# Kernel tuning notes

Measured on AMD Instinct MI355X. Metric: run time of the kernel, lower is better.

## Reference

```python
import jax, jax.numpy as jnp
import numpy as np

CHUNK = 32  # config.scan_chunk_size


def setup_inputs() -> dict:
    key = jax.random.key(0)
    ks = jax.random.split(key, 12)
    B, T, D, SD, OD = 8, 2048, 512, 256, 64
    w = lambda i, shape: (jax.random.normal(ks[i], shape, dtype=jnp.float32) * 0.02)
    return {
        "x": jax.random.normal(ks[0], (B, T, D), dtype=jnp.float32),
        "gate_W": w(1, (D, SD)), "gate_b": jnp.zeros((SD,), jnp.float32),
        "in_W": w(2, (D, SD)), "in_b": jnp.zeros((SD,), jnp.float32),
        "out_W": w(3, (SD, D)), "out_b": jnp.zeros((D,), jnp.float32),
        "opv_W": w(4, (D, OD)), "opv_b": jnp.zeros((OD,), jnp.float32),
        "opk_W": w(5, (D, OD)), "opk_b": jnp.zeros((OD,), jnp.float32),
        "opq_W": w(6, (D, OD)), "opq_b": jnp.zeros((OD,), jnp.float32),
        "op_decay": jnp.full((OD,), 0.95, jnp.float32),
        "opout_W": w(7, (OD, D)), "opout_b": jnp.zeros((D,), jnp.float32),
        "ln_g": jnp.ones((D,), jnp.float32), "ln_b": jnp.zeros((D,), jnp.float32),
    }


def _chunked_scan(gates, drive, K):
    # gates, drive: [B,T,SD]; T divisible by K
    B, T, SD = drive.shape
    nC = T // K
    a = gates.reshape(B, nC, K, SD)
    b = drive.reshape(B, nC, K, SD)
    log_cum_a = jnp.cumsum(jnp.log(jnp.maximum(a, 1e-6)), axis=2)
    cum_a = jnp.exp(log_cum_a)                               # [B,nC,K,SD]
    cum_wb = jnp.cumsum(b / jnp.maximum(cum_a, 1e-8), axis=2)
    # sequential scan over chunks to propagate the carry h
    def step(h, inputs):
        ca_last, wb_last = inputs                            # [B,SD] each
        h_new = ca_last * (h + wb_last)
        return h_new, h                                      # emit h BEFORE this chunk
    h0 = jnp.zeros((B, SD), drive.dtype)
    _, h_prev = jax.lax.scan(
        step, h0,
        (cum_a[:, :, -1].transpose(1, 0, 2), cum_wb[:, :, -1].transpose(1, 0, 2)))
    h_prev = h_prev.transpose(1, 0, 2)                       # [B,nC,SD]
    states = cum_a * (h_prev[:, :, None, :] + cum_wb)
    return states.reshape(B, T, SD)


def _binding_scan_outer(v, k, q, decay):
    # v,k,q: [B,T,OD]; S_t = diag(decay) @ S_{t-1} + v_t k_t^T; o_t = S_t q_t
    B, T, OD = v.shape
    def step(S, vkq):
        vt, kt, qt = vkq                                     # [B,OD] each
        S_new = decay[None, :, None] * S + vt[:, :, None] * kt[:, None, :]
        o = jnp.einsum('bij,bj->bi', S_new, qt)
        return S_new, o
    S0 = jnp.zeros((B, OD, OD), v.dtype)
    _, outs = jax.lax.scan(step, S0, (v.transpose(1, 0, 2), k.transpose(1, 0, 2), q.transpose(1, 0, 2)))
    return outs.transpose(1, 0, 2)                           # [B,T,OD]


def reference(x, gate_W, gate_b, in_W, in_b, out_W, out_b,
              opv_W, opv_b, opk_W, opk_b, opq_W, opq_b, op_decay,
              opout_W, opout_b, ln_g, ln_b):
    gates = jax.nn.sigmoid(x @ gate_W + gate_b)              # [B,T,SD]
    drive = (1.0 - gates) * (x @ in_W + in_b)
    states = _chunked_scan(gates, drive, CHUNK)
    scan_out = states @ out_W + out_b                        # [B,T,D]
    # binding scan (mode='outer')
    v = x @ opv_W + opv_b
    k = x @ opk_W + opk_b
    q = x @ opq_W + opq_b
    dec = jax.nn.sigmoid(op_decay)
    bind = _binding_scan_outer(v, k, q, dec) @ opout_W + opout_b
    y = x + scan_out + bind
    mu = jnp.mean(y, axis=-1, keepdims=True)
    var = jnp.mean((y - mu) ** 2, axis=-1, keepdims=True)
    return (y - mu) / jnp.sqrt(var + 1e-5) * ln_g + ln_b
```

## Files before the change

### kernel.cpp

```cpp
#include <hip/hip_runtime.h>
#include <hip/hip_bf16.h>
#include <hip/hip_fp16.h>
#include <math.h>

#define BB 8
#define TT 2048
#define DD 512
#define SD 256
#define OD 64
#define CHUNK 32
#define NC 64
#define CB 64
#define NCB 32
#define MM (BB*TT)
#define KCAT 320

typedef __attribute__((ext_vector_type(8))) short bf16x8_t;
typedef __attribute__((ext_vector_type(4))) float f32x4;

__device__ __forceinline__ void gload_lds16(const void* gsrc, void* ldst) {
    __builtin_amdgcn_global_load_lds(
        (const __attribute__((address_space(1))) unsigned int*)gsrc,
        (__attribute__((address_space(3))) unsigned int*)ldst,
        16, 0, 0);
}

__device__ __forceinline__ float4 ldh4(const __half* p) {
    __half2 a = *(const __half2*)p;
    __half2 b = *(const __half2*)(p + 2);
    float2 fa = __half22float2(a), fb = __half22float2(b);
    return make_float4(fa.x, fa.y, fb.x, fb.y);
}

__global__ __launch_bounds__(256) void conv_w(
    const float* __restrict__ gate_W, const float* __restrict__ gate_b,
    const float* __restrict__ in_W,   const float* __restrict__ in_b,
    const float* __restrict__ opv_W,  const float* __restrict__ opk_W,
    const float* __restrict__ opq_W,
    const float* __restrict__ opv_b,  const float* __restrict__ opk_b,
    const float* __restrict__ opq_b,
    __hip_bfloat16* __restrict__ Wcat, float* __restrict__ bias_cat)
{
    int idx = blockIdx.x * 256 + threadIdx.x;
    if (idx < 393216) {
        int n = idx >> 9, k = idx & 511;
        float v;
        if (n < 256)       v = gate_W[k * 256 + n];
        else if (n < 512)  v = in_W[k * 256 + (n - 256)];
        else if (n < 704) {
            int h = (n - 512) >> 6, j = (n - 512) & 63;
            const float* W = (h == 0) ? opv_W : (h == 1) ? opk_W : opq_W;
            v = W[k * 64 + j];
        } else v = 0.f;
        Wcat[idx] = __float2bfloat16(v);
        return;
    }
    idx -= 393216;
    if (idx < 768) {
        float v;
        if (idx < 256)      v = gate_b[idx];
        else if (idx < 512) v = in_b[idx - 256];
        else if (idx < 704) {
            int h = (idx - 512) >> 6, j = (idx - 512) & 63;
            v = (h == 0) ? opv_b[j] : (h == 1) ? opk_b[j] : opq_b[j];
        } else v = 0.f;
        bias_cat[idx] = v;
    }
}

__global__ __launch_bounds__(512, 6) void gemm_proj(
    const float* __restrict__ A,
    const __hip_bfloat16* __restrict__ Bt,
    const float* __restrict__ bias,
    __half* __restrict__ out0,
    __half* __restrict__ out1,
    int M, int N, int K, int n0, int sigCols)
{
    constexpr int BM = 128, BK = 32;
    __shared__ alignas(16) __hip_bfloat16 Abuf[3][BM * BK];
    __shared__ alignas(16) __hip_bfloat16 Bbuf[3][BM * BK];
    const int tid = threadIdx.x;
    const int lane = tid & 63, wid = tid >> 6;
    const int wr = wid >> 2, wc = wid & 3;
    const int nbn = N >> 7;
    const int chunk = gridDim.x >> 3;
    const int b = blockIdx.x;
    const int orig = (b & 7) * chunk + (b >> 3);
    const int bm = (orig / nbn) * BM, bn = (orig % nbn) * BM;
    const int l15 = lane & 15, hgr = lane >> 4;

    const int grow = tid >> 2, gslot = tid & 3;
    const int gsw = gslot ^ ((grow >> 1) & 3);
    const float* srcA = A + (size_t)(bm + grow) * K + gslot * 8;
    const int wOffA = grow * 64 + gsw * 16;
    const __hip_bfloat16* srcB = Bt + (size_t)(bn + grow) * K + gsw * 8;
    const int ldsOffB = (tid & ~63) * 16;

    int offA[4], offB[2];
    #pragma unroll
    for (int mi = 0; mi < 4; ++mi) {
        int r = wr * 64 + mi * 16 + l15;
        offA[mi] = r * 64 + (hgr ^ ((r >> 1) & 3)) * 16;
    }
    #pragma unroll
    for (int nj = 0; nj < 2; ++nj) {
        int r = wc * 32 + nj * 16 + l15;
        offB[nj] = r * 64 + (hgr ^ ((r >> 1) & 3)) * 16;
    }

    f32x4 acc[4][2] = {};
    const int nk = K / BK;
    float4 pA0, pA1, qA0, qA1;

#define WRITE_A(IDX, R0, R1) do { \
        alignas(16) __hip_bfloat16 h_[8] = { \
            __float2bfloat16((R0).x), __float2bfloat16((R0).y), \
            __float2bfloat16((R0).z), __float2bfloat16((R0).w), \
            __float2bfloat16((R1).x), __float2bfloat16((R1).y), \
            __float2bfloat16((R1).z), __float2bfloat16((R1).w)}; \
        *(float4*)((char*)&Abuf[(IDX)][0] + wOffA) = *(float4*)h_; \
    } while (0)

#define FRAG_MFMA(T) do { \
        const char* ab_ = (const char*)&Abuf[(T) % 3][0]; \
        const char* bb_ = (const char*)&Bbuf[(T) % 3][0]; \
        bf16x8_t af_[4], bf_[2]; \
        _Pragma("unroll") \
        for (int mi = 0; mi < 4; ++mi) af_[mi] = *(const bf16x8_t*)(ab_ + offA[mi]); \
        _Pragma("unroll") \
        for (int nj = 0; nj < 2; ++nj) bf_[nj] = *(const bf16x8_t*)(bb_ + offB[nj]); \
        _Pragma("unroll") \
        for (int mi = 0; mi < 4; ++mi) \
            _Pragma("unroll") \
            for (int nj = 0; nj < 2; ++nj) \
                acc[mi][nj] = __builtin_amdgcn_mfma_f32_16x16x32_bf16( \
                    af_[mi], bf_[nj], acc[mi][nj], 0, 0, 0); \
    } while (0)

#define GEMM_STEP(T, I0, I1, W0, W1) do { \
        int k2_ = ((T) + 2) * BK; \
        I0 = *(const float4*)(srcA + k2_); \
        I1 = *(const float4*)(srcA + k2_ + 4); \
        gload_lds16(srcB + k2_, (char*)&Bbuf[((T) + 2) % 3][0] + ldsOffB); \
        FRAG_MFMA(T); \
        WRITE_A(((T) + 1) % 3, W0, W1); \
        asm volatile("s_waitcnt vmcnt(3) lgkmcnt(0)" ::: "memory"); \
        __builtin_amdgcn_sched_barrier(0); \
        __builtin_amdgcn_s_barrier(); \
        __builtin_amdgcn_sched_barrier(0); \
    } while (0)

    pA0 = *(const float4*)(srcA);
    pA1 = *(const float4*)(srcA + 4);
    gload_lds16(srcB, (char*)&Bbuf[0][0] + ldsOffB);
    qA0 = *(const float4*)(srcA + BK);
    qA1 = *(const float4*)(srcA + BK + 4);
    gload_lds16(srcB + BK, (char*)&Bbuf[1][0] + ldsOffB);
    asm volatile("s_waitcnt vmcnt(3)" ::: "memory");
    WRITE_A(0, pA0, pA1);
    asm volatile("s_waitcnt lgkmcnt(0)" ::: "memory");
    __builtin_amdgcn_sched_barrier(0);
    __builtin_amdgcn_s_barrier();
    __builtin_amdgcn_sched_barrier(0);

    for (int tt = 0; tt + 3 < nk; tt += 2) {
        GEMM_STEP(tt,     pA0, pA1, qA0, qA1);
        GEMM_STEP(tt + 1, qA0, qA1, pA0, pA1);
    }
    FRAG_MFMA(nk - 2);
    WRITE_A((nk - 1) % 3, qA0, qA1);
    __syncthreads();
    FRAG_MFMA(nk - 1);

#undef GEMM_STEP
#undef FRAG_MFMA
#undef WRITE_A

    const int n1 = N - n0;
    #pragma unroll
    for (int mi = 0; mi < 4; ++mi) {
        #pragma unroll
        for (int nj = 0; nj < 2; ++nj) {
            int col = bn + wc * 32 + nj * 16 + l15;
            int r0 = bm + wr * 64 + mi * 16 + hgr * 4;
            float bv = bias[col];
            #pragma unroll
            for (int e = 0; e < 4; ++e) {
                int row = r0 + e;
                float val = acc[mi][nj][e] + bv;
                if (col < n0) {
                    if (col < sigCols) val = 1.f / (1.f + expf(-val));
                    out0[(size_t)row * n0 + col] = __float2half(val);
                } else {
                    out1[(size_t)row * n1 + (col - n0)] = __float2half(val);
                }
            }
        }
    }
}

__device__ void scan_pass1_body(int blk,
    const __half* __restrict__ gi,
    float* __restrict__ ca_last, float* __restrict__ wb_last)
{
    int idx = blk * 256 + threadIdx.x;
    int sd = idx & 255;
    int c  = (idx >> 8) & 63;
    int b  = idx >> 14;
    size_t base = ((size_t)(b * TT + c * CHUNK)) * 512;
    float prod = 1.f, wb = 0.f;
    for (int i = 0; i < CHUNK; ++i) {
        size_t off = base + (size_t)i * 512;
        float g  = __half2float(gi[off + sd]);
        float il = __half2float(gi[off + 256 + sd]);
        float a = fmaxf(g, 1e-6f);
        prod *= a;
        wb += (1.f - g) * il / fmaxf(prod, 1e-8f);
    }
    int cidx = (b * NC + c) * SD + sd;
    ca_last[cidx] = prod;
    wb_last[cidx] = wb;
}

__device__ void scan_pass3_body(int blk,
    const __half* __restrict__ gi, const float* __restrict__ h_prev,
    __hip_bfloat16* __restrict__ cat)
{
    int idx = blk * 256 + threadIdx.x;
    int sd = idx & 255;
    int c  = (idx >> 8) & 63;
    int b  = idx >> 14;
    size_t base = ((size_t)(b * TT + c * CHUNK)) * 512;
    size_t obase = ((size_t)(b * TT + c * CHUNK)) * KCAT + sd;
    float h = h_prev[(b * NC + c) * SD + sd];
    float prod = 1.f, wb = 0.f;
    for (int i = 0; i < CHUNK; ++i) {
        size_t off = base + (size_t)i * 512;
        float g  = __half2float(gi[off + sd]);
        float il = __half2float(gi[off + 256 + sd]);
        float a = fmaxf(g, 1e-6f);
        prod *= a;
        wb += (1.f - g) * il / fmaxf(prod, 1e-8f);
        cat[obase + (size_t)i * KCAT] = __float2bfloat16(prod * (h + wb));
    }
}

#define LST 68
__device__ void bind_p1_body(int bc,
    const __half* __restrict__ vkq, const float* __restrict__ op_decay,
    float* __restrict__ o, float* __restrict__ dS,
    float* B1, float* B2, float* B3, float* l2d)
{
    const int b = bc >> 5, c = bc & 31;
    const size_t base = ((size_t)b * TT + (size_t)c * CB) * 256;
    const size_t obase = ((size_t)b * TT + (size_t)c * CB) * OD;
    const int tid = threadIdx.x;
    if (tid < 64) l2d[tid] = log2f(1.f / (1.f + expf(-op_decay[tid])));
    const int lr = tid >> 4, lc = (tid & 15) << 2;
    #pragma unroll
    for (int rr = 0; rr < 4; ++rr) {
        int t = lr + rr * 16;
        float4 qv = ldh4(&vkq[base + t * 256 + 128 + lc]);
        float4 kv = ldh4(&vkq[base + t * 256 + 64 + lc]);
        float q4[4] = {qv.x, qv.y, qv.z, qv.w};
        float k4[4] = {kv.x, kv.y, kv.z, kv.w};
        #pragma unroll
        for (int j = 0; j < 4; ++j) {
            B1[(lc + j) * LST + t] = q4[j];
            B2[(lc + j) * LST + t] = k4[j];
        }
    }
    __syncthreads();
    const int tx = tid & 15, ty = tid >> 4;
    {
        float a_acc[4][4] = {};
        for (int d = 0; d < 64; ++d) {
            float4 q4 = *(const float4*)&B1[d * LST + 4 * ty];
            float4 k4 = *(const float4*)&B2[d * LST + 4 * tx];
            float qr[4] = {q4.x, q4.y, q4.z, q4.w};
            float kr[4] = {k4.x, k4.y, k4.z, k4.w};
            #pragma unroll
            for (int r = 0; r < 4; ++r)
                #pragma unroll
                for (int s = 0; s < 4; ++s)
                    a_acc[r][s] = fmaf(qr[r], kr[s], a_acc[r][s]);
        }
        __syncthreads();
        #pragma unroll
        for (int s = 0; s < 4; ++s) {
            int ss = 4 * tx + s;
            float w[4];
            #pragma unroll
            for (int r = 0; r < 4; ++r)
                w[r] = (ss <= 4 * ty + r) ? a_acc[r][s] : 0.f;
            *(float4*)&B3[ss * LST + 4 * ty] = *(float4*)w;
        }
    }
    #pragma unroll
    for (int rr = 0; rr < 4; ++rr) {
        int m = lr + rr * 16;
        float4 vv = ldh4(&vkq[base + m * 256 + 0 + lc]);
        float4 kv = ldh4(&vkq[base + m * 256 + 64 + lc]);
        float v4[4] = {vv.x, vv.y, vv.z, vv.w};
        #pragma unroll
        for (int j = 0; j < 4; ++j)
            v4[j] *= exp2f(-(float)m * l2d[lc + j]);
        *(float4*)&B1[m * LST + lc] = *(float4*)v4;
        float k4[4] = {kv.x, kv.y, kv.z, kv.w};
        *(float4*)&B2[m * LST + lc] = *(float4*)k4;
    }
    __syncthreads();
    {
        float p[4][4] = {};
        for (int s = 0; s < 64; ++s) {
            float4 a4 = *(const float4*)&B3[s * LST + 4 * ty];
            float4 v4 = *(const float4*)&B1[s * LST + 4 * tx];
            float ar[4] = {a4.x, a4.y, a4.z, a4.w};
            float vr[4] = {v4.x, v4.y, v4.z, v4.w};
            #pragma unroll
            for (int r = 0; r < 4; ++r)
                #pragma unroll
                for (int i2 = 0; i2 < 4; ++i2)
                    p[r][i2] = fmaf(ar[r], vr[i2], p[r][i2]);
        }
        #pragma unroll
        for (int r = 0; r < 4; ++r) {
            int t = 4 * ty + r;
            float w[4];
            #pragma unroll
            for (int i2 = 0; i2 < 4; ++i2)
                w[i2] = exp2f((float)t * l2d[4 * tx + i2]) * p[r][i2];
            *(float4*)&o[obase + t * OD + 4 * tx] = *(float4*)w;
        }
    }
    {
        float sacc[4][4] = {};
        for (int m = 0; m < 64; ++m) {
            float4 v4 = *(const float4*)&B1[m * LST + 4 * ty];
            float4 k4 = *(const float4*)&B2[m * LST + 4 * tx];
            float vr[4] = {v4.x, v4.y, v4.z, v4.w};
            float kr[4] = {k4.x, k4.y, k4.z, k4.w};
            #pragma unroll
            for (int r = 0; r < 4; ++r)
                #pragma unroll
                for (int j = 0; j < 4; ++j)
                    sacc[r][j] = fmaf(vr[r], kr[j], sacc[r][j]);
        }
        float* dSb = dS + (size_t)bc * 4096;
        #pragma unroll
        for (int r = 0; r < 4; ++r) {
            int i = 4 * ty + r;
            float scale = exp2f(63.f * l2d[i]);
            float w[4];
            #pragma unroll
            for (int j2 = 0; j2 < 4; ++j2)
                w[j2] = scale * sacc[r][j2];
            *(float4*)&dSb[i * 64 + 4 * tx] = *(float4*)w;
        }
    }
}

__device__ void bind_p3_body(int bc,
    const __half* __restrict__ vkq, const float* __restrict__ Sstart,
    const float* __restrict__ op_decay, const float* __restrict__ o,
    __hip_bfloat16* __restrict__ cat,
    float* B1, float* B2, float* l2d)
{
    const int b = bc >> 5, c = bc & 31;
    const size_t base = ((size_t)b * TT + (size_t)c * CB) * 256;
    const size_t obase = ((size_t)b * TT + (size_t)c * CB) * OD;
    const size_t cbase = ((size_t)b * TT + (size_t)c * CB) * KCAT + 256;
    const int tid = threadIdx.x;
    if (tid < 64) l2d[tid] = log2f(1.f / (1.f + expf(-op_decay[tid])));
    const int lr = tid >> 4, lc = (tid & 15) << 2;
    const float* Sb = Sstart + (size_t)bc * 4096;
    #pragma unroll
    for (int rr = 0; rr < 4; ++rr) {
        int t = lr + rr * 16;
        float4 qv = ldh4(&vkq[base + t * 256 + 128 + lc]);
        float4 sv = *(const float4*)&Sb[t * 64 + lc];
        float q4[4] = {qv.x, qv.y, qv.z, qv.w};
        float s4[4] = {sv.x, sv.y, sv.z, sv.w};
        #pragma unroll
        for (int j = 0; j < 4; ++j) {
            B1[(lc + j) * LST + t] = q4[j];
            B2[(lc + j) * LST + t] = s4[j];
        }
    }
    __syncthreads();
    const int tx = tid & 15, ty = tid >> 4;
    float acc[4][4] = {};
    for (int j = 0; j < 64; ++j) {
        float4 q4 = *(const float4*)&B1[j * LST + 4 * ty];
        float4 s4 = *(const float4*)&B2[j * LST + 4 * tx];
        float qr[4] = {q4.x, q4.y, q4.z, q4.w};
        float sr[4] = {s4.x, s4.y, s4.z, s4.w};
        #pragma unroll
        for (int r = 0; r < 4; ++r)
            #pragma unroll
            for (int i2 = 0; i2 < 4; ++i2)
                acc[r][i2] = fmaf(qr[r], sr[i2], acc[r][i2]);
    }
    #pragma unroll
    for (int r = 0; r < 4; ++r) {
        int l = 4 * ty + r;
        alignas(8) __hip_bfloat16 w[4];
        #pragma unroll
        for (int i2 = 0; i2 < 4; ++i2) {
            int i = 4 * tx + i2;
            float val = o[obase + l * OD + i] + exp2f((float)(l + 1) * l2d[i]) * acc[r][i2];
            w[i2] = __float2bfloat16(val);
        }
        *(float2*)&cat[cbase + l * KCAT + 4 * tx] = *(float2*)w;
    }
}

__global__ __launch_bounds__(256) void fused1(
    const __half* __restrict__ gi, const __half* __restrict__ vkq,
    const float* __restrict__ op_decay,
    float* __restrict__ ca_last, float* __restrict__ wb_last,
    float* __restrict__ o_intra, float* __restrict__ dS)
{
    __shared__ float B1[64 * LST];
    __shared__ float B2[64 * LST];
    __shared__ float B3[64 * LST];
    __shared__ float l2d[64];
    const int bid = blockIdx.x;
    if (bid < 256) bind_p1_body(bid, vkq, op_decay, o_intra, dS, B1, B2, B3, l2d);
    else           scan_pass1_body(bid - 256, gi, ca_last, wb_last);
}

__global__ __launch_bounds__(256) void fused2(
    const float* __restrict__ dS, const float* __restrict__ op_decay,
    float* __restrict__ Sstart,
    const float* __restrict__ ca_last, const float* __restrict__ wb_last,
    float* __restrict__ h_prev,
    const float* __restrict__ out_W, const float* __restrict__ out_b,
    const float* __restrict__ opout_W, const float* __restrict__ opout_b,
    __hip_bfloat16* __restrict__ Wcomb, float* __restrict__ bias_comb)
{
    const int bid = blockIdx.x;
    if (bid < 128) {
        int idx = bid * 256 + threadIdx.x;
        int j = idx & 63, i = (idx >> 6) & 63, b = idx >> 12;
        float dec = 1.f / (1.f + expf(-op_decay[i]));
        float d64 = exp2f(64.f * log2f(dec));
        float S = 0.f;
        for (int c = 0; c < NCB; ++c) {
            size_t o = (((size_t)b * NCB + c) * 4096) + i * 64 + j;
            Sstart[o] = S;
            S = d64 * S + dS[o];
        }
    } else if (bid < 136) {
        int idx = (bid - 128) * 256 + threadIdx.x;
        int sd = idx & 255;
        int b  = idx >> 8;
        float h = 0.f;
        for (int c = 0; c < NC; ++c) {
            int o = (b * NC + c) * SD + sd;
            h_prev[o] = h;
            h = ca_last[o] * (h + wb_last[o]);
        }
    } else {
        int idx = (bid - 136) * 256 + threadIdx.x;
        if (idx < 163840) {
            int n = idx / KCAT, k = idx % KCAT;
            float v = (k < 256) ? out_W[k * 512 + n] : opout_W[(k - 256) * 512 + n];
            Wcomb[idx] = __float2bfloat16(v);
            return;
        }
        idx -= 163840;
        if (idx < 512) bias_comb[idx] = out_b[idx] + opout_b[idx];
    }
}

__global__ __launch_bounds__(256) void fused3(
    const __half* __restrict__ gi, const float* __restrict__ h_prev,
    const __half* __restrict__ vkq, const float* __restrict__ Sstart,
    const float* __restrict__ op_decay, const float* __restrict__ o_intra,
    __hip_bfloat16* __restrict__ cat)
{
    __shared__ float B1[64 * LST];
    __shared__ float B2[64 * LST];
    __shared__ float l2d[64];
    const int bid = blockIdx.x;
    if (bid < 256) bind_p3_body(bid, vkq, Sstart, op_decay, o_intra, cat, B1, B2, l2d);
    else           scan_pass3_body(bid - 256, gi, h_prev, cat);
}

__global__ __launch_bounds__(512) void outgemm_ln(
    const __hip_bfloat16* __restrict__ cat,
    const __hip_bfloat16* __restrict__ Wcomb,
    const float* __restrict__ bias_comb,
    const float* __restrict__ x,
    const float* __restrict__ lng, const float* __restrict__ lnb,
    float* __restrict__ y)
{
    constexpr int BM = 32, BK = 32, NN = 512;
    __shared__ alignas(16) __hip_bfloat16 As[2][BM * BK];
    __shared__ alignas(16) __hip_bfloat16 Bs[2][NN * BK];
    __shared__ float psum[8][BM], psum2[8][BM], mvmu[BM], mvrs[BM];
    const int tid = threadIdx.x;
    const int lane = tid & 63, wid = tid >> 6;
    const int l15 = lane & 15, hgr = lane >> 4;
    const int bm = blockIdx.x * BM;

    const __hip_bfloat16* srcA = cat;
    int ldsOffA = 0;
    {
        int gg = (wid & 1) * 64 + lane;
        int row = gg >> 2, sl = (gg & 3) ^ ((row >> 1) & 3);
        srcA = cat + (size_t)(bm + row) * KCAT + sl * 8;
        ldsOffA = (wid & 1) * 1024;
    }
    const __hip_bfloat16* srcB[4];
    int ldsOffB[4];
    #pragma unroll
    for (int c = 0; c < 4; ++c) {
        int gg = (wid * 4 + c) * 64 + lane;
        int row = gg >> 2, sl = (gg & 3) ^ ((row >> 1) & 3);
        srcB[c] = Wcomb + (size_t)row * KCAT + sl * 8;
        ldsOffB[c] = (wid * 4 + c) * 1024;
    }
    int offA[2], offB[4];
    #pragma unroll
    for (int mi = 0; mi < 2; ++mi) {
        int r = mi * 16 + l15;
        offA[mi] = r * 64 + (hgr ^ ((r >> 1) & 3)) * 16;
    }
    #pragma unroll
    for (int nj = 0; nj < 4; ++nj) {
        int n = wid * 64 + nj * 16 + l15;
        offB[nj] = n * 64 + (hgr ^ ((n >> 1) & 3)) * 16;
    }

    f32x4 acc[2][4] = {};
    constexpr int nk = KCAT / BK;

    if (wid < 2) gload_lds16(srcA, (char*)&As[0][0] + ldsOffA);
    #pragma unroll
    for (int c = 0; c < 4; ++c) gload_lds16(srcB[c], (char*)&Bs[0][0] + ldsOffB[c]);
    __syncthreads();

    int cur = 0;
    for (int t = 0; t < nk; ++t) {
        if (t + 1 < nk) {
            int k0 = (t + 1) * BK;
            if (wid < 2) gload_lds16(srcA + k0, (char*)&As[cur ^ 1][0] + ldsOffA);
            #pragma unroll
            for (int c = 0; c < 4; ++c)
                gload_lds16(srcB[c] + k0, (char*)&Bs[cur ^ 1][0] + ldsOffB[c]);
        }
        bf16x8_t af[2], bfr[4];
        #pragma unroll
        for (int mi = 0; mi < 2; ++mi)
            af[mi] = *(const bf16x8_t*)((const char*)&As[cur][0] + offA[mi]);
        #pragma unroll
        for (int nj = 0; nj < 4; ++nj)
            bfr[nj] = *(const bf16x8_t*)((const char*)&Bs[cur][0] + offB[nj]);
        #pragma unroll
        for (int mi = 0; mi < 2; ++mi)
            #pragma unroll
            for (int nj = 0; nj < 4; ++nj)
                acc[mi][nj] = __builtin_amdgcn_mfma_f32_16x16x32_bf16(
                    af[mi], bfr[nj], acc[mi][nj], 0, 0, 0);
        __syncthreads();
        cur ^= 1;
    }

    #pragma unroll
    for (int nj = 0; nj < 4; ++nj) {
        int col = wid * 64 + nj * 16 + l15;
        float bc_ = bias_comb[col];
        #pragma unroll
        for (int mi = 0; mi < 2; ++mi) {
            int r0 = bm + mi * 16 + hgr * 4;
            #pragma unroll
            for (int e = 0; e < 4; ++e)
                acc[mi][nj][e] += bc_ + x[(size_t)(r0 + e) * DD + col];
        }
    }
    float s[8], s2[8];
    #pragma unroll
    for (int mi = 0; mi < 2; ++mi)
        #pragma unroll
        for (int e = 0; e < 4; ++e) {
            float a = 0.f, b2 = 0.f;
            #pragma unroll
            for (int nj = 0; nj < 4; ++nj) {
                float v = acc[mi][nj][e];
                a += v; b2 += v * v;
            }
            s[mi * 4 + e] = a; s2[mi * 4 + e] = b2;
        }
    #pragma unroll
    for (int off = 1; off <= 8; off <<= 1)
        #pragma unroll
        for (int i = 0; i < 8; ++i) {
            s[i]  += __shfl_xor(s[i], off);
            s2[i] += __shfl_xor(s2[i], off);
        }
    if (l15 == 0) {
        #pragma unroll
        for (int mi = 0; mi < 2; ++mi)
            #pragma unroll
            for (int e = 0; e < 4; ++e) {
                int lr = mi * 16 + hgr * 4 + e;
                psum[wid][lr]  = s[mi * 4 + e];
                psum2[wid][lr] = s2[mi * 4 + e];
            }
    }
    __syncthreads();
    if (tid < BM) {
        float tot = 0.f, tot2 = 0.f;
        #pragma unroll
        for (int w2 = 0; w2 < 8; ++w2) { tot += psum[w2][tid]; tot2 += psum2[w2][tid]; }
        float mu = tot * (1.f / 512.f);
        float var = tot2 * (1.f / 512.f) - mu * mu;
        mvmu[tid] = mu;
        mvrs[tid] = rsqrtf(var + 1e-5f);
    }
    __syncthreads();
    #pragma unroll
    for (int nj = 0; nj < 4; ++nj) {
        int col = wid * 64 + nj * 16 + l15;
        float g = lng[col], bb = lnb[col];
        #pragma unroll
        for (int mi = 0; mi < 2; ++mi) {
            #pragma unroll
            for (int e = 0; e < 4; ++e) {
                int lr = mi * 16 + hgr * 4 + e;
                y[(size_t)(bm + lr) * DD + col] =
                    (acc[mi][nj][e] - mvmu[lr]) * mvrs[lr] * g + bb;
            }
        }
    }
}

extern "C" void kernel_launch(void* const* d_in, const int* in_sizes, int n_in,
                              void* d_out, int out_size, void* d_ws, size_t ws_size,
                              hipStream_t stream)
{
    const float* x       = (const float*)d_in[0];
    const float* gate_W  = (const float*)d_in[1];
    const float* gate_b  = (const float*)d_in[2];
    const float* in_W    = (const float*)d_in[3];
    const float* in_b    = (const float*)d_in[4];
    const float* out_W   = (const float*)d_in[5];
    const float* out_b   = (const float*)d_in[6];
    const float* opv_W   = (const float*)d_in[7];
    const float* opv_b   = (const float*)d_in[8];
    const float* opk_W   = (const float*)d_in[9];
    const float* opk_b   = (const float*)d_in[10];
    const float* opq_W   = (const float*)d_in[11];
    const float* opq_b   = (const float*)d_in[12];
    const float* op_dec  = (const float*)d_in[13];
    const float* opout_W = (const float*)d_in[14];
    const float* opout_b = (const float*)d_in[15];
    const float* ln_g    = (const float*)d_in[16];
    const float* ln_b    = (const float*)d_in[17];
    float* y = (float*)d_out;

    char* w = (char*)d_ws;
    auto alloc = [&](size_t bytes) { char* p = w; w += (bytes + 255) & ~(size_t)255; return p; };
    __half* gi       = (__half*)alloc((size_t)MM * 512 * 2);
    __half* vkq      = (__half*)alloc((size_t)MM * 256 * 2);
    float* o_intra   = (float*)alloc((size_t)MM * 64 * 4);
    float* ca_last   = (float*)alloc((size_t)BB * NC * SD * 4);
    float* wb_last   = (float*)alloc((size_t)BB * NC * SD * 4);
    float* h_prev    = (float*)alloc((size_t)BB * NC * SD * 4);
    float* dS        = (float*)alloc((size_t)BB * NCB * 4096 * 4);
    float* Sstart    = (float*)alloc((size_t)BB * NCB * 4096 * 4);
    float* bias_cat  = (float*)alloc(768 * 4);
    float* bias_comb = (float*)alloc(512 * 4);
    __hip_bfloat16* cat   = (__hip_bfloat16*)alloc((size_t)MM * KCAT * 2);
    __hip_bfloat16* Wcat  = (__hip_bfloat16*)alloc((size_t)768 * 512 * 2);
    __hip_bfloat16* Wcomb = (__hip_bfloat16*)alloc((size_t)512 * KCAT * 2);

    hipLaunchKernelGGL(conv_w, dim3((393216 + 768 + 255) / 256), dim3(256), 0, stream,
                       gate_W, gate_b, in_W, in_b, opv_W, opk_W, opq_W,
                       opv_b, opk_b, opq_b, Wcat, bias_cat);
    hipLaunchKernelGGL(gemm_proj, dim3(6 * (MM / 128)), dim3(512), 0, stream,
                       x, Wcat, bias_cat, gi, vkq,
                       MM, 768, 512, 512, 256);
    hipLaunchKernelGGL(fused1, dim3(768), dim3(256), 0, stream,
                       gi, vkq, op_dec, ca_last, wb_last, o_intra, dS);
    hipLaunchKernelGGL(fused2, dim3(136 + (163840 + 512 + 255) / 256), dim3(256), 0, stream,
                       dS, op_dec, Sstart, ca_last, wb_last, h_prev,
                       out_W, out_b, opout_W, opout_b, Wcomb, bias_comb);
    hipLaunchKernelGGL(fused3, dim3(768), dim3(256), 0, stream,
                       gi, h_prev, vkq, Sstart, op_dec, o_intra, cat);
    hipLaunchKernelGGL(outgemm_ln, dim3(MM / 32), dim3(512), 0, stream,
                       cat, Wcomb, bias_comb, x, ln_g, ln_b, y);
}
```

Measured before the change: 87.61 us.

## Deepen gemm_proj prefetch pipeline to three tiles ahead with four B buffers

Restructures the projection GEMM's software pipeline so global loads are issued three K-tiles ahead instead of two. B now uses a 4-deep LDS ring and A a 2-deep ring, with a third register pair holding prefetched A. The loop is hardcoded for nk=16 (K=512) and the waitcnt thresholds are adjusted. The aim is to hide more global-memory latency, at the cost of more LDS and registers, which may reduce occupancy. It also breaks generality for other K values.

```diff
diff --git a/kernel.cpp b/kernel.cpp
--- a/kernel.cpp
+++ b/kernel.cpp
@@ -77,8 +77,8 @@
     int M, int N, int K, int n0, int sigCols)
 {
     constexpr int BM = 128, BK = 32;
-    __shared__ alignas(16) __hip_bfloat16 Abuf[3][BM * BK];
-    __shared__ alignas(16) __hip_bfloat16 Bbuf[3][BM * BK];
+    __shared__ alignas(16) __hip_bfloat16 Abuf[2][BM * BK];
+    __shared__ alignas(16) __hip_bfloat16 Bbuf[4][BM * BK];
     const int tid = threadIdx.x;
     const int lane = tid & 63, wid = tid >> 6;
     const int wr = wid >> 2, wc = wid & 3;
@@ -110,7 +110,7 @@
 
     f32x4 acc[4][2] = {};
     const int nk = K / BK;
-    float4 pA0, pA1, qA0, qA1;
+    float4 pA0, pA1, qA0, qA1, rA0, rA1;
 
 #define WRITE_A(IDX, R0, R1) do { \
         alignas(16) __hip_bfloat16 h_[8] = { \
@@ -122,8 +122,8 @@
     } while (0)
 
 #define FRAG_MFMA(T) do { \
-        const char* ab_ = (const char*)&Abuf[(T) % 3][0]; \
-        const char* bb_ = (const char*)&Bbuf[(T) % 3][0]; \
+        const char* ab_ = (const char*)&Abuf[(T) & 1][0]; \
+        const char* bb_ = (const char*)&Bbuf[(T) & 3][0]; \
         bf16x8_t af_[4], bf_[2]; \
         _Pragma("unroll") \
         for (int mi = 0; mi < 4; ++mi) af_[mi] = *(const bf16x8_t*)(ab_ + offA[mi]); \
@@ -137,14 +137,17 @@
                     af_[mi], bf_[nj], acc[mi][nj], 0, 0, 0); \
     } while (0)
 
-#define GEMM_STEP(T, I0, I1, W0, W1) do { \
-        int k2_ = ((T) + 2) * BK; \
-        I0 = *(const float4*)(srcA + k2_); \
-        I1 = *(const float4*)(srcA + k2_ + 4); \
-        gload_lds16(srcB + k2_, (char*)&Bbuf[((T) + 2) % 3][0] + ldsOffB); \
+#define ISSUE3(T, I0, I1) do { \
+        int k3_ = ((T) + 3) * BK; \
+        I0 = *(const float4*)(srcA + k3_); \
+        I1 = *(const float4*)(srcA + k3_ + 4); \
+        gload_lds16(srcB + k3_, (char*)&Bbuf[((T) + 3) & 3][0] + ldsOffB); \
+    } while (0)
+
+#define STEP_TAIL(T, W0, W1, VMLINE) do { \
         FRAG_MFMA(T); \
-        WRITE_A(((T) + 1) % 3, W0, W1); \
-        asm volatile("s_waitcnt vmcnt(3) lgkmcnt(0)" ::: "memory"); \
+        WRITE_A(((T) + 1) & 1, W0, W1); \
+        asm volatile(VMLINE ::: "memory"); \
         __builtin_amdgcn_sched_barrier(0); \
         __builtin_amdgcn_s_barrier(); \
         __builtin_amdgcn_sched_barrier(0); \
@@ -156,23 +159,31 @@
     qA0 = *(const float4*)(srcA + BK);
     qA1 = *(const float4*)(srcA + BK + 4);
     gload_lds16(srcB + BK, (char*)&Bbuf[1][0] + ldsOffB);
-    asm volatile("s_waitcnt vmcnt(3)" ::: "memory");
+    rA0 = *(const float4*)(srcA + 2 * BK);
+    rA1 = *(const float4*)(srcA + 2 * BK + 4);
+    gload_lds16(srcB + 2 * BK, (char*)&Bbuf[2][0] + ldsOffB);
     WRITE_A(0, pA0, pA1);
-    asm volatile("s_waitcnt lgkmcnt(0)" ::: "memory");
+    asm volatile("s_waitcnt vmcnt(6) lgkmcnt(0)" ::: "memory");
     __builtin_amdgcn_sched_barrier(0);
     __builtin_amdgcn_s_barrier();
     __builtin_amdgcn_sched_barrier(0);
 
-    for (int tt = 0; tt + 3 < nk; tt += 2) {
-        GEMM_STEP(tt,     pA0, pA1, qA0, qA1);
-        GEMM_STEP(tt + 1, qA0, qA1, pA0, pA1);
-    }
-    FRAG_MFMA(nk - 2);
-    WRITE_A((nk - 1) % 3, qA0, qA1);
-    __syncthreads();
-    FRAG_MFMA(nk - 1);
-
-#undef GEMM_STEP
+    for (int tt = 0; tt < 12; tt += 3) {
+        ISSUE3(tt, pA0, pA1);
+        STEP_TAIL(tt, qA0, qA1, "s_waitcnt vmcnt(6) lgkmcnt(0)");
+        ISSUE3(tt + 1, qA0, qA1);
+        STEP_TAIL(tt + 1, rA0, rA1, "s_waitcnt vmcnt(6) lgkmcnt(0)");
+        ISSUE3(tt + 2, rA0, rA1);
+        STEP_TAIL(tt + 2, pA0, pA1, "s_waitcnt vmcnt(6) lgkmcnt(0)");
+    }
+    ISSUE3(12, pA0, pA1);
+    STEP_TAIL(12, qA0, qA1, "s_waitcnt vmcnt(6) lgkmcnt(0)");
+    STEP_TAIL(13, rA0, rA1, "s_waitcnt vmcnt(3) lgkmcnt(0)");
+    STEP_TAIL(14, pA0, pA1, "s_waitcnt vmcnt(0) lgkmcnt(0)");
+    FRAG_MFMA(15);
+
+#undef STEP_TAIL
+#undef ISSUE3
 #undef FRAG_MFMA
 #undef WRITE_A
 
```

Measured after the change: 89.23 us. Within noise of the previous version (+1.9%).
